# Performance work log

Hardware: AMD Instinct MI355X
Metric: run time of the kernel (lower is better)

The kernel has to match this reference:

```python
import jax, jax.numpy as jnp
import numpy as np

D_MODEL = 1024
NUM_HEADS = 16
HEAD_DIM = D_MODEL // NUM_HEADS  # 64
B, S = 2, 2048


def setup_inputs() -> dict:
    key = jax.random.key(0)
    k1, k2, k3, k4, k5 = jax.random.split(key, 5)
    scale = 1.0 / np.sqrt(D_MODEL)
    return {
        "x": jax.random.normal(k1, (B, S, D_MODEL), dtype=jnp.float32),
        "Wq": jax.random.normal(k2, (D_MODEL, D_MODEL), dtype=jnp.float32) * scale,
        "bq": jax.random.normal(k3, (D_MODEL,), dtype=jnp.float32) * 0.02,
        "Wv": jax.random.normal(k4, (D_MODEL, D_MODEL), dtype=jnp.float32) * scale,
        "bv": jax.random.normal(k5, (D_MODEL,), dtype=jnp.float32) * 0.02,
    }


def reference(x, Wq, bq, Wv, bv):
    b, s, _ = x.shape
    d, n = HEAD_DIM, NUM_HEADS
    # nn.Linear: y = x @ W.T + b
    Q = x @ Wq.T + bq
    # NOTE (faithful to source bug): K uses the VALUE projection, key weights unused.
    KV = x @ Wv.T + bv
    # einops 'B S (d n) -> B S d n' -> 'B n S d'  (head index n is fast-varying)
    Qh = Q.reshape(b, s, d, n).transpose(0, 3, 1, 2)   # [B, n, S, d]
    Kt = KV.reshape(b, s, d, n).transpose(0, 3, 2, 1)  # [B, n, d, S]
    Vh = KV.reshape(b, s, d, n).transpose(0, 3, 1, 2)  # [B, n, S, d]
    scores = jnp.matmul(Qh, Kt) / jnp.sqrt(jnp.float32(d))  # [B, n, S, S]
    attn = jnp.matmul(jax.nn.softmax(scores, axis=-1), Vh)  # [B, n, S, d]
    # 'B n S d -> B S (n d)'
    out = attn.transpose(0, 2, 1, 3).reshape(b, s, n * d)
    return out
```

## Files before the change

kernel.cpp:

```cpp
#include <hip/hip_runtime.h>
#include <hip/hip_bf16.h>
#include <math.h>


typedef __bf16 bf16x8 __attribute__((ext_vector_type(8)));
typedef float  f32x4  __attribute__((ext_vector_type(4)));
typedef short  s16x4  __attribute__((ext_vector_type(4)));
typedef unsigned short ushort_t;
typedef unsigned short us8 __attribute__((ext_vector_type(8)));

#define QSCALE 0.1803368801111204f

__device__ __forceinline__ unsigned short f2bf(float f) {
  unsigned int u = __builtin_bit_cast(unsigned int, f);
  u += 0x7fffu + ((u >> 16) & 1u);
  return (unsigned short)(u >> 16);
}

__device__ __forceinline__ unsigned int pk2(float a, float b) {
  unsigned int ua = __builtin_bit_cast(unsigned int, a) + 0x8000u;
  unsigned int ub = __builtin_bit_cast(unsigned int, b) + 0x8000u;
  return (ua >> 16) | (ub & 0xffff0000u);
}

__device__ __forceinline__ void gl_lds16(const void* g, void* l) {
  __builtin_amdgcn_global_load_lds(
      (const __attribute__((address_space(1))) unsigned int*)g,
      (__attribute__((address_space(3))) unsigned int*)l, 16, 0, 0);
}

__device__ __forceinline__ f32x4 mfma_k32(bf16x8 a, bf16x8 b, f32x4 c) {
  return __builtin_amdgcn_mfma_f32_16x16x32_bf16(a, b, c, 0, 0, 0);
}
__device__ __forceinline__ f32x4 mfma_k16(s16x4 a, s16x4 b, f32x4 c) {
  return __builtin_amdgcn_mfma_f32_16x16x16bf16_1k(a, b, c, 0, 0, 0);
}

__global__ __launch_bounds__(256) void cvt3_kernel(const float4* __restrict__ x,
                                                   const float4* __restrict__ wq,
                                                   const float4* __restrict__ wv,
                                                   ushort4* __restrict__ dst) {
  const int i = blockIdx.x * 256 + threadIdx.x;
  const float4 v = (i < 1048576) ? x[i]
                 : (i < 1310720) ? wq[i - 1048576]
                                 : wv[i - 1310720];
  ushort4 o;
  o.x = f2bf(v.x); o.y = f2bf(v.y); o.z = f2bf(v.z); o.w = f2bf(v.w);
  dst[i] = o;
}

__global__ __launch_bounds__(256) void proj_kernel(
    const ushort_t* __restrict__ X,
    const ushort_t* __restrict__ Wqm,
    const ushort_t* __restrict__ Wvm,
    const float*    __restrict__ bq,
    const float*    __restrict__ bv,
    ushort_t* __restrict__ Qh,
    ushort_t* __restrict__ KVh)
{
  __shared__ __align__(16) unsigned char lds[32768];
  const int tid = threadIdx.x;
  const int w  = tid >> 6;
  const int l  = tid & 63;
  const int lq = l >> 4;
  const int ll = l & 15;
  const bool isQ = (blockIdx.z == 0);
  const ushort_t* Wmat = isQ ? Wqm : Wvm;
  const float*    bias = isQ ? bq  : bv;
  const int m0 = blockIdx.x * 128;
  const int by = blockIdx.y;
  const int wm = (w & 1) * 64;
  const int wn = (w >> 1) * 64;

  f32x4 acc[4][4] = {};

  for (int k0 = 0; k0 < 1024; k0 += 64) {
    __syncthreads();
#pragma unroll
    for (int t = 0; t < 4; ++t) {
      const int seg = w * 4 + t;
      const int r = seg * 8 + (l >> 3);
      const int cd = (l & 7) ^ (r & 7);
      const int cg = by * 128 + r;
      const int wrow = ((cg & 63) << 4) | (cg >> 6);
      gl_lds16(X    + (size_t)(m0 + r) * 1024 + k0 + cd * 8, lds + seg * 1024);
      gl_lds16(Wmat + (size_t)wrow * 1024 + k0 + cd * 8, lds + 16384 + seg * 1024);
    }
    __syncthreads();
#pragma unroll
    for (int kb = 0; kb < 2; ++kb) {
      const int kc = kb * 4 + lq;
      bf16x8 af[4], bfr[4];
#pragma unroll
      for (int mi = 0; mi < 4; ++mi) {
        const int m = wm + mi * 16 + ll;
        af[mi] = *(const bf16x8*)(lds + m * 128 + ((kc ^ (m & 7)) * 16));
      }
#pragma unroll
      for (int ni = 0; ni < 4; ++ni) {
        const int n = wn + ni * 16 + ll;
        bfr[ni] = *(const bf16x8*)(lds + 16384 + n * 128 + ((kc ^ (n & 7)) * 16));
      }
#pragma unroll
      for (int mi = 0; mi < 4; ++mi)
#pragma unroll
        for (int ni = 0; ni < 4; ++ni)
          acc[mi][ni] = mfma_k32(af[mi], bfr[ni], acc[mi][ni]);
    }
  }

  const int hh = (by * 128 + wn) >> 6;
#pragma unroll
  for (int ni = 0; ni < 4; ++ni) {
    const int ii = ni * 16 + ll;
    const float bb = bias[(ii << 4) | hh];
#pragma unroll
    for (int mi = 0; mi < 4; ++mi) {
#pragma unroll
      for (int r = 0; r < 4; ++r) {
        const int row = m0 + wm + mi * 16 + lq * 4 + r;
        const int b = row >> 11, s = row & 2047;
        const float v = acc[mi][ni][r] + bb;
        const size_t idx = (((size_t)(b * 16 + hh)) * 2048 + s) * 64 + ii;
        if (isQ) Qh[idx] = f2bf(v * QSCALE);
        else     KVh[idx] = f2bf(v);
      }
    }
  }
}

__global__ __launch_bounds__(256) void tr_kernel(const ushort_t* __restrict__ KVh,
                                                 ushort_t* __restrict__ KVt) {
  __shared__ __align__(16) ushort_t t[64 * 128];
  const int tid = threadIdx.x;
  const int bh = blockIdx.y;
  const int s0 = blockIdx.x * 128;
  const ushort_t* src = KVh + ((size_t)bh * 2048 + s0) * 64;
  const int d0 = (tid & 7) * 8;
#pragma unroll
  for (int u0 = 0; u0 < 64; u0 += 32) {
    const int u = u0 + (tid >> 3);
    us8 ra = *(const us8*)(src + (size_t)(2 * u) * 64 + d0);
    us8 rb = *(const us8*)(src + (size_t)(2 * u + 1) * 64 + d0);
#pragma unroll
    for (int j = 0; j < 8; ++j) {
      const int d = d0 + j;
      const int cs = (u >> 2) ^ (d & 15);
      *(unsigned int*)&t[d * 128 + cs * 8 + (u & 3) * 2] =
          (unsigned int)ra[j] | ((unsigned int)rb[j] << 16);
    }
  }
  __syncthreads();
  ushort_t* dst = KVt + (size_t)bh * 64 * 2048 + s0;
  const int d = tid >> 2;
#pragma unroll
  for (int p = 0; p < 4; ++p) {
    const int c = (tid & 3) + p * 4;
    const int cs = c ^ (d & 15);
    us8 v = *(const us8*)&t[d * 128 + cs * 8];
    *(us8*)(dst + (size_t)d * 2048 + c * 8) = v;
  }
}

__global__ __launch_bounds__(256, 4) void attn_kernel(
    const ushort_t* __restrict__ Qh,
    const ushort_t* __restrict__ KVh,
    const ushort_t* __restrict__ KVt,
    float* __restrict__ out)
{
  __shared__ __align__(16) unsigned char sm[32768];
  const int tid = threadIdx.x;
  const int w  = tid >> 6;
  const int l  = tid & 63;
  const int quad = l >> 4;
  const int ll = l & 15;
  const int bid = blockIdx.x;
  const int bh = ((bid & 7) << 2) | (bid >> 8);
  const int qt = (bid >> 3) & 31;
  const int b = bh >> 4, h = bh & 15;
  const int qw = qt * 64 + w * 16;
  const ushort_t* Qhead  = Qh  + (size_t)bh * (2048 * 64);
  const ushort_t* Khead  = KVh + (size_t)bh * (2048 * 64);
  const ushort_t* Vthead = KVt + (size_t)bh * (64 * 2048);

  bf16x8 qf[2];
#pragma unroll
  for (int kb = 0; kb < 2; ++kb)
    qf[kb] = *(const bf16x8*)(Qhead + (size_t)(qw + ll) * 64 + kb * 32 + quad * 8);

  f32x4 O[4] = {};
  float l_run = 0.f;

  for (int kt = 0; kt < 16; ++kt) {
    const int sk0 = kt * 128;
    __syncthreads();
#pragma unroll
    for (int t = 0; t < 4; ++t) {
      const int seg = w * 4 + t;
      const int r = seg * 8 + (l >> 3);
      const int cd = (l & 7) ^ (r & 7);
      gl_lds16(Khead + (size_t)(sk0 + r) * 64 + cd * 8, sm + seg * 1024);
    }
#pragma unroll
    for (int t = 0; t < 4; ++t) {
      const int seg = w * 4 + t;
      const int d = seg * 4 + (l >> 4);
      const int c8 = (l & 15) ^ (d & 15);
      gl_lds16(Vthead + (size_t)d * 2048 + sk0 + c8 * 8, sm + 16384 + seg * 1024);
    }
    __syncthreads();

    f32x4 Sa[8] = {};
#pragma unroll
    for (int kb = 0; kb < 2; ++kb) {
      const int kc = kb * 4 + quad;
#pragma unroll
      for (int ni = 0; ni < 8; ++ni) {
        const int n = ni * 16 + ll;
        const bf16x8 ak = *(const bf16x8*)(sm + n * 128 + ((kc ^ (n & 7)) * 16));
        Sa[ni] = mfma_k32(ak, qf[kb], Sa[ni]);
      }
    }

    float ps = 0.f;
    s16x4 pk[8];
#pragma unroll
    for (int ni = 0; ni < 8; ++ni) {
      const float p0 = __builtin_amdgcn_exp2f(Sa[ni][0]);
      const float p1 = __builtin_amdgcn_exp2f(Sa[ni][1]);
      const float p2 = __builtin_amdgcn_exp2f(Sa[ni][2]);
      const float p3 = __builtin_amdgcn_exp2f(Sa[ni][3]);
      ps += (p0 + p1) + (p2 + p3);
      const uint2 uu = make_uint2(pk2(p0, p1), pk2(p2, p3));
      pk[ni] = __builtin_bit_cast(s16x4, uu);
    }
    ps += __shfl_xor(ps, 16);
    ps += __shfl_xor(ps, 32);
    l_run += ps;

#pragma unroll
    for (int ni = 0; ni < 8; ++ni) {
      const int cb = 2 * ni + (quad >> 1);
#pragma unroll
      for (int no = 0; no < 4; ++no) {
        const int row = no * 16 + ll;
        const s16x4 bv = *(const s16x4*)(sm + 16384 + row * 256 +
                                         ((cb ^ ll) * 16) + (quad & 1) * 8);
        O[no] = mfma_k16(pk[ni], bv, O[no]);
      }
    }
  }

  const float inv = 1.f / l_run;
  float invr[4];
#pragma unroll
  for (int r = 0; r < 4; ++r)
    invr[r] = __shfl(inv, (l & 48) + ((l & 48) >> 2) + r);

  float* op = out + ((size_t)(b * 2048) + qw) * 1024 + h * 64;
#pragma unroll
  for (int no = 0; no < 4; ++no)
#pragma unroll
    for (int r = 0; r < 4; ++r) {
      const int q = quad * 4 + r;
      op[(size_t)q * 1024 + no * 16 + ll] = O[no][r] * invr[r];
    }
}

extern "C" void kernel_launch(void* const* d_in, const int* in_sizes, int n_in,
                              void* d_out, int out_size, void* d_ws, size_t ws_size,
                              hipStream_t stream) {
  const float* x  = (const float*)d_in[0];
  const float* Wq = (const float*)d_in[1];
  const float* bq = (const float*)d_in[2];
  const float* Wv = (const float*)d_in[3];
  const float* bv = (const float*)d_in[4];
  float* out = (float*)d_out;
  char* ws = (char*)d_ws;

  ushort_t* xbf  = (ushort_t*)(ws);
  ushort_t* wqbf = (ushort_t*)(ws + 8388608);
  ushort_t* wvbf = (ushort_t*)(ws + 10485760);
  ushort_t* Qh   = (ushort_t*)(ws + 12582912);
  ushort_t* KVh  = (ushort_t*)(ws + 20971520);
  ushort_t* KVt  = (ushort_t*)(ws + 29360128);

  cvt3_kernel<<<6144, 256, 0, stream>>>((const float4*)x, (const float4*)Wq,
                                        (const float4*)Wv, (ushort4*)xbf);
  proj_kernel<<<dim3(32, 8, 2), 256, 0, stream>>>(xbf, wqbf, wvbf, bq, bv, Qh, KVh);
  tr_kernel<<<dim3(16, 32), 256, 0, stream>>>(KVh, KVt);
  attn_kernel<<<1024, 256, 0, stream>>>(Qh, KVh, KVt, out);
}
```

Measured before the change: 161.5 us.

## Double-buffer K/V tiles and process two query chunks per wave in attention

```diff
diff --git a/kernel.cpp b/kernel.cpp
--- a/kernel.cpp
+++ b/kernel.cpp
@@ -162,109 +162,143 @@
   }
 }
 
-__global__ __launch_bounds__(256, 4) void attn_kernel(
+__global__ __launch_bounds__(256, 2) void attn_kernel(
     const ushort_t* __restrict__ Qh,
     const ushort_t* __restrict__ KVh,
     const ushort_t* __restrict__ KVt,
     float* __restrict__ out)
 {
-  __shared__ __align__(16) unsigned char sm[32768];
+  __shared__ __align__(16) unsigned char sm[65536];
   const int tid = threadIdx.x;
   const int w  = tid >> 6;
   const int l  = tid & 63;
   const int quad = l >> 4;
   const int ll = l & 15;
   const int bid = blockIdx.x;
-  const int bh = ((bid & 7) << 2) | (bid >> 8);
-  const int qt = (bid >> 3) & 31;
+  const int bh = ((bid & 7) << 2) | (bid >> 7);
+  const int qt = (bid >> 3) & 15;
   const int b = bh >> 4, h = bh & 15;
-  const int qw = qt * 64 + w * 16;
+  const int qbase = qt * 128 + w * 32;
   const ushort_t* Qhead  = Qh  + (size_t)bh * (2048 * 64);
   const ushort_t* Khead  = KVh + (size_t)bh * (2048 * 64);
   const ushort_t* Vthead = KVt + (size_t)bh * (64 * 2048);
 
-  bf16x8 qf[2];
-#pragma unroll
-  for (int kb = 0; kb < 2; ++kb)
-    qf[kb] = *(const bf16x8*)(Qhead + (size_t)(qw + ll) * 64 + kb * 32 + quad * 8);
-
-  f32x4 O[4] = {};
-  float l_run = 0.f;
+  bf16x8 qf[2][2];
+#pragma unroll
+  for (int c = 0; c < 2; ++c)
+#pragma unroll
+    for (int kb = 0; kb < 2; ++kb)
+      qf[c][kb] = *(const bf16x8*)(Qhead + (size_t)(qbase + c * 16 + ll) * 64 +
+                                   kb * 32 + quad * 8);
+
+  const int ksegr = (w * 4) * 8 + (l >> 3);
+  const int kcd   = (l & 7);
+#pragma unroll
+  for (int t = 0; t < 4; ++t) {
+    const int seg = w * 4 + t;
+    const int r = seg * 8 + (l >> 3);
+    const int cd = (l & 7) ^ (r & 7);
+    gl_lds16(Khead + (size_t)r * 64 + cd * 8, sm + seg * 1024);
+  }
+#pragma unroll
+  for (int t = 0; t < 4; ++t) {
+    const int seg = w * 4 + t;
+    const int d = seg * 4 + (l >> 4);
+    const int k16 = ((l & 15) - 2 * d) & 15;
+    gl_lds16(Vthead + (size_t)d * 2048 + k16 * 8, sm + 32768 + seg * 1024);
+  }
+
+  f32x4 O[2][4] = {};
+  float l_run[2] = {0.f, 0.f};
 
   for (int kt = 0; kt < 16; ++kt) {
     const int sk0 = kt * 128;
+    const int buf = kt & 1;
     __syncthreads();
-#pragma unroll
-    for (int t = 0; t < 4; ++t) {
-      const int seg = w * 4 + t;
-      const int r = seg * 8 + (l >> 3);
-      const int cd = (l & 7) ^ (r & 7);
-      gl_lds16(Khead + (size_t)(sk0 + r) * 64 + cd * 8, sm + seg * 1024);
-    }
-#pragma unroll
-    for (int t = 0; t < 4; ++t) {
-      const int seg = w * 4 + t;
-      const int d = seg * 4 + (l >> 4);
-      const int c8 = (l & 15) ^ (d & 15);
-      gl_lds16(Vthead + (size_t)d * 2048 + sk0 + c8 * 8, sm + 16384 + seg * 1024);
-    }
-    __syncthreads();
-
-    f32x4 Sa[8] = {};
+
+    if (kt < 15) {
+      const int bo = (buf ^ 1) * 16384;
+#pragma unroll
+      for (int t = 0; t < 4; ++t) {
+        const int seg = w * 4 + t;
+        const int r = seg * 8 + (l >> 3);
+        const int cd = (l & 7) ^ (r & 7);
+        gl_lds16(Khead + (size_t)(sk0 + 128 + r) * 64 + cd * 8, sm + bo + seg * 1024);
+      }
+#pragma unroll
+      for (int t = 0; t < 4; ++t) {
+        const int seg = w * 4 + t;
+        const int d = seg * 4 + (l >> 4);
+        const int k16 = ((l & 15) - 2 * d) & 15;
+        gl_lds16(Vthead + (size_t)d * 2048 + sk0 + 128 + k16 * 8,
+                 sm + 32768 + bo + seg * 1024);
+      }
+    }
+    const unsigned char* Kb = sm + buf * 16384;
+    const unsigned char* Vb = sm + 32768 + buf * 16384;
+
+    f32x4 Sa[2][8] = {};
 #pragma unroll
     for (int kb = 0; kb < 2; ++kb) {
       const int kc = kb * 4 + quad;
 #pragma unroll
       for (int ni = 0; ni < 8; ++ni) {
         const int n = ni * 16 + ll;
-        const bf16x8 ak = *(const bf16x8*)(sm + n * 128 + ((kc ^ (n & 7)) * 16));
-        Sa[ni] = mfma_k32(ak, qf[kb], Sa[ni]);
-      }
-    }
-
-    float ps = 0.f;
-    s16x4 pk[8];
+        const bf16x8 ak = *(const bf16x8*)(Kb + n * 128 + ((kc ^ (n & 7)) * 16));
+        Sa[0][ni] = mfma_k32(ak, qf[0][kb], Sa[0][ni]);
+        Sa[1][ni] = mfma_k32(ak, qf[1][kb], Sa[1][ni]);
+      }
+    }
+
+    s16x4 pk[2][8];
+#pragma unroll
+    for (int c = 0; c < 2; ++c) {
+      float ps = 0.f;
+#pragma unroll
+      for (int ni = 0; ni < 8; ++ni) {
+        const float p0 = __builtin_amdgcn_exp2f(Sa[c][ni][0]);
+        const float p1 = __builtin_amdgcn_exp2f(Sa[c][ni][1]);
+        const float p2 = __builtin_amdgcn_exp2f(Sa[c][ni][2]);
+        const float p3 = __builtin_amdgcn_exp2f(Sa[c][ni][3]);
+        ps += (p0 + p1) + (p2 + p3);
+        const uint2 uu = make_uint2(pk2(p0, p1), pk2(p2, p3));
+        pk[c][ni] = __builtin_bit_cast(s16x4, uu);
+      }
+      ps += __shfl_xor(ps, 16);
+      ps += __shfl_xor(ps, 32);
+      l_run[c] += ps;
+    }
+
 #pragma unroll
     for (int ni = 0; ni < 8; ++ni) {
-      const float p0 = __builtin_amdgcn_exp2f(Sa[ni][0]);
-      const float p1 = __builtin_amdgcn_exp2f(Sa[ni][1]);
-      const float p2 = __builtin_amdgcn_exp2f(Sa[ni][2]);
-      const float p3 = __builtin_amdgcn_exp2f(Sa[ni][3]);
-      ps += (p0 + p1) + (p2 + p3);
-      const uint2 uu = make_uint2(pk2(p0, p1), pk2(p2, p3));
-      pk[ni] = __builtin_bit_cast(s16x4, uu);
-    }
-    ps += __shfl_xor(ps, 16);
-    ps += __shfl_xor(ps, 32);
-    l_run += ps;
-
-#pragma unroll
-    for (int ni = 0; ni < 8; ++ni) {
-      const int cb = 2 * ni + (quad >> 1);
 #pragma unroll
       for (int no = 0; no < 4; ++no) {
-        const int row = no * 16 + ll;
-        const s16x4 bv = *(const s16x4*)(sm + 16384 + row * 256 +
-                                         ((cb ^ ll) * 16) + (quad & 1) * 8);
-        O[no] = mfma_k16(pk[ni], bv, O[no]);
-      }
-    }
-  }
-
-  const float inv = 1.f / l_run;
-  float invr[4];
-#pragma unroll
-  for (int r = 0; r < 4; ++r)
-    invr[r] = __shfl(inv, (l & 48) + ((l & 48) >> 2) + r);
-
-  float* op = out + ((size_t)(b * 2048) + qw) * 1024 + h * 64;
-#pragma unroll
-  for (int no = 0; no < 4; ++no)
-#pragma unroll
-    for (int r = 0; r < 4; ++r) {
-      const int q = quad * 4 + r;
-      op[(size_t)q * 1024 + no * 16 + ll] = O[no][r] * invr[r];
-    }
+        const int d = no * 16 + ll;
+        const s16x4 bv = *(const s16x4*)(Vb + d * 256 +
+                                         ((4 * ni + quad + 4 * ll) & 31) * 8);
+        O[0][no] = mfma_k16(pk[0][ni], bv, O[0][no]);
+        O[1][no] = mfma_k16(pk[1][ni], bv, O[1][no]);
+      }
+    }
+  }
+  (void)ksegr; (void)kcd;
+
+#pragma unroll
+  for (int c = 0; c < 2; ++c) {
+    const float inv = 1.f / l_run[c];
+    float invr[4];
+#pragma unroll
+    for (int r = 0; r < 4; ++r)
+      invr[r] = __shfl(inv, (l & 48) + ((l & 48) >> 2) + r);
+    float* op = out + ((size_t)(b * 2048) + qbase + c * 16) * 1024 + h * 64;
+#pragma unroll
+    for (int no = 0; no < 4; ++no)
+#pragma unroll
+      for (int r = 0; r < 4; ++r) {
+        const int q = quad * 4 + r;
+        op[(size_t)q * 1024 + no * 16 + ll] = O[c][no][r] * invr[r];
+      }
+  }
 }
 
 extern "C" void kernel_launch(void* const* d_in, const int* in_sizes, int n_in,
@@ -289,5 +323,5 @@
                                         (const float4*)Wv, (ushort4*)xbf);
   proj_kernel<<<dim3(32, 8, 2), 256, 0, stream>>>(xbf, wqbf, wvbf, bq, bv, Qh, KVh);
   tr_kernel<<<dim3(16, 32), 256, 0, stream>>>(KVh, KVt);
-  attn_kernel<<<1024, 256, 0, stream>>>(Qh, KVh, KVt, out);
-}
+  attn_kernel<<<512, 256, 0, stream>>>(Qh, KVh, KVt, out);
+}
```

Result: no change. 162.8 us (+0.8%).

## Fuse KV transpose into projection epilogue via LDS staging

Applied to the files above, without the earlier changes.

```diff
diff --git a/kernel.cpp b/kernel.cpp
--- a/kernel.cpp
+++ b/kernel.cpp
@@ -56,7 +56,8 @@
     const float*    __restrict__ bq,
     const float*    __restrict__ bv,
     ushort_t* __restrict__ Qh,
-    ushort_t* __restrict__ KVh)
+    ushort_t* __restrict__ KVh,
+    ushort_t* __restrict__ KVt)
 {
   __shared__ __align__(16) unsigned char lds[32768];
   const int tid = threadIdx.x;
@@ -109,56 +110,63 @@
     }
   }
 
-  const int hh = (by * 128 + wn) >> 6;
-#pragma unroll
-  for (int ni = 0; ni < 4; ++ni) {
-    const int ii = ni * 16 + ll;
-    const float bb = bias[(ii << 4) | hh];
-#pragma unroll
-    for (int mi = 0; mi < 4; ++mi) {
-#pragma unroll
-      for (int r = 0; r < 4; ++r) {
-        const int row = m0 + wm + mi * 16 + lq * 4 + r;
-        const int b = row >> 11, s = row & 2047;
-        const float v = acc[mi][ni][r] + bb;
-        const size_t idx = (((size_t)(b * 16 + hh)) * 2048 + s) * 64 + ii;
-        if (isQ) Qh[idx] = f2bf(v * QSCALE);
-        else     KVh[idx] = f2bf(v);
-      }
-    }
-  }
-}
-
-__global__ __launch_bounds__(256) void tr_kernel(const ushort_t* __restrict__ KVh,
-                                                 ushort_t* __restrict__ KVt) {
-  __shared__ __align__(16) ushort_t t[64 * 128];
-  const int tid = threadIdx.x;
-  const int bh = blockIdx.y;
-  const int s0 = blockIdx.x * 128;
-  const ushort_t* src = KVh + ((size_t)bh * 2048 + s0) * 64;
-  const int d0 = (tid & 7) * 8;
-#pragma unroll
-  for (int u0 = 0; u0 < 64; u0 += 32) {
-    const int u = u0 + (tid >> 3);
-    us8 ra = *(const us8*)(src + (size_t)(2 * u) * 64 + d0);
-    us8 rb = *(const us8*)(src + (size_t)(2 * u + 1) * 64 + d0);
-#pragma unroll
-    for (int j = 0; j < 8; ++j) {
-      const int d = d0 + j;
-      const int cs = (u >> 2) ^ (d & 15);
-      *(unsigned int*)&t[d * 128 + cs * 8 + (u & 3) * 2] =
-          (unsigned int)ra[j] | ((unsigned int)rb[j] << 16);
-    }
-  }
-  __syncthreads();
-  ushort_t* dst = KVt + (size_t)bh * 64 * 2048 + s0;
-  const int d = tid >> 2;
-#pragma unroll
-  for (int p = 0; p < 4; ++p) {
-    const int c = (tid & 3) + p * 4;
-    const int cs = c ^ (d & 15);
-    us8 v = *(const us8*)&t[d * 128 + cs * 8];
-    *(us8*)(dst + (size_t)d * 2048 + c * 8) = v;
+  const int hl = wn >> 6;
+  const int hh = by * 2 + hl;
+  const int b  = m0 >> 11;
+  const int sbase = m0 & 2047;
+
+  if (isQ) {
+#pragma unroll
+    for (int ni = 0; ni < 4; ++ni) {
+      const int ii = ni * 16 + ll;
+      const float bb = bias[(ii << 4) | hh];
+#pragma unroll
+      for (int mi = 0; mi < 4; ++mi)
+#pragma unroll
+        for (int r = 0; r < 4; ++r) {
+          const int s = sbase + wm + mi * 16 + lq * 4 + r;
+          const float v = acc[mi][ni][r] + bb;
+          Qh[(((size_t)(b * 16 + hh)) * 2048 + s) * 64 + ii] = f2bf(v * QSCALE);
+        }
+    }
+  } else {
+    __syncthreads();
+#pragma unroll
+    for (int ni = 0; ni < 4; ++ni) {
+      const int ii = ni * 16 + ll;
+      const float bb = bias[(ii << 4) | hh];
+#pragma unroll
+      for (int mi = 0; mi < 4; ++mi) {
+        const float v0 = acc[mi][ni][0] + bb;
+        const float v1 = acc[mi][ni][1] + bb;
+        const float v2 = acc[mi][ni][2] + bb;
+        const float v3 = acc[mi][ni][3] + bb;
+        const unsigned int u01 = pk2(v0, v1);
+        const unsigned int u23 = pk2(v2, v3);
+        const int sl = wm + mi * 16 + lq * 4;
+        const size_t kb0 = (((size_t)(b * 16 + hh)) * 2048 + sbase + sl) * 64 + ii;
+        KVh[kb0]       = (ushort_t)(u01 & 0xffffu);
+        KVh[kb0 + 64]  = (ushort_t)(u01 >> 16);
+        KVh[kb0 + 128] = (ushort_t)(u23 & 0xffffu);
+        KVh[kb0 + 192] = (ushort_t)(u23 >> 16);
+        const int g = (wm >> 2) + mi * 4 + lq;
+        const int pc = (g >> 1) ^ ll;
+        *(uint2*)(lds + hl * 16384 + ii * 256 + pc * 16 + (g & 1) * 8) =
+            make_uint2(u01, u23);
+      }
+    }
+    __syncthreads();
+    const int row = tid >> 1;
+    const int hl2 = row >> 6, ii2 = row & 63;
+    const int cbase = (tid & 1) * 8;
+    ushort_t* dst = KVt + (((size_t)(b * 16 + by * 2 + hl2)) * 64 + ii2) * 2048 + sbase;
+#pragma unroll
+    for (int cc = 0; cc < 8; ++cc) {
+      const int c = cbase + cc;
+      const int pc = c ^ (ii2 & 15);
+      const us8 v = *(const us8*)(lds + hl2 * 16384 + ii2 * 256 + pc * 16);
+      *(us8*)(dst + c * 8) = v;
+    }
   }
 }
 
@@ -287,7 +295,7 @@
 
   cvt3_kernel<<<6144, 256, 0, stream>>>((const float4*)x, (const float4*)Wq,
                                         (const float4*)Wv, (ushort4*)xbf);
-  proj_kernel<<<dim3(32, 8, 2), 256, 0, stream>>>(xbf, wqbf, wvbf, bq, bv, Qh, KVh);
-  tr_kernel<<<dim3(16, 32), 256, 0, stream>>>(KVh, KVt);
+  proj_kernel<<<dim3(32, 8, 2), 256, 0, stream>>>(xbf, wqbf, wvbf, bq, bv,
+                                                  Qh, KVh, KVt);
   attn_kernel<<<1024, 256, 0, stream>>>(Qh, KVh, KVt, out);
 }
```

Measured after the change: 157.7 us. -2.4%, faster.
